# Performance work log

Hardware: AMD Instinct MI355X
Metric: run time of the kernel (lower is better)

Reference implementation:

```python
import jax, jax.numpy as jnp
import numpy as np

N_NODES = 50000
N_EDGES = 800000
N_RELS = 65
D = 64
N_GRAPHS = 512


def setup_inputs() -> dict:
    key = jax.random.key(0)
    ks = jax.random.split(key, 20)
    inp = {
        "node_feats": jax.random.normal(ks[0], (N_NODES, D), dtype=jnp.float32),
        "etypes": jax.random.randint(ks[1], (N_EDGES,), 0, N_RELS),
        "src": jax.random.randint(ks[2], (N_EDGES,), 0, N_NODES),
        "dst": jax.random.randint(ks[3], (N_EDGES,), 0, N_NODES),
        "graph_ids": jnp.sort(jax.random.randint(ks[4], (N_NODES,), 0, N_GRAPHS)),
    }
    s = 1.0 / np.sqrt(D)
    # 3 RGCN layers: per-relation weights (basis with num_bases=num_rels == full) + bias
    for i, k in zip(range(1, 4), (ks[5], ks[6], ks[7])):
        inp[f"W_rel{i}"] = jax.random.normal(k, (N_RELS, D, D), dtype=jnp.float32) * s
        inp[f"b{i}"] = jnp.zeros((D,), dtype=jnp.float32)
    # 3 FC layers
    for i, k in zip(range(1, 4), (ks[8], ks[9], ks[10])):
        inp[f"fc_W{i}"] = jax.random.normal(k, (D, D), dtype=jnp.float32) * s
        inp[f"fc_b{i}"] = jnp.zeros((D,), dtype=jnp.float32)
    inp["pred_W"] = jax.random.normal(ks[11], (D, 2), dtype=jnp.float32) * s
    inp["pred_b"] = jnp.zeros((2,), dtype=jnp.float32)
    return inp


def _rgcn_layer(h, W, b, etypes, src, dst):
    # all-relation projection: [N, R, K]
    proj = jnp.einsum('nd,rdk->nrk', h, W)
    # per-edge gather of relation-specific message: [E, K]
    msg = proj[src, etypes]
    # scatter-sum into destination nodes
    agg = jax.ops.segment_sum(msg, dst, num_segments=h.shape[0])
    return jax.nn.relu(agg + b)


def reference(node_feats, etypes, src, dst, graph_ids,
              W_rel1, b1, W_rel2, b2, W_rel3, b3,
              fc_W1, fc_b1, fc_W2, fc_b2, fc_W3, fc_b3,
              pred_W, pred_b):
    h = node_feats
    h = _rgcn_layer(h, W_rel1, b1, etypes, src, dst)
    h = _rgcn_layer(h, W_rel2, b2, etypes, src, dst)
    h = _rgcn_layer(h, W_rel3, b3, etypes, src, dst)
    # sum-pool nodes per graph: [G, D]
    g = jax.ops.segment_sum(h, graph_ids, num_segments=N_GRAPHS)
    g = jax.nn.relu(g @ fc_W1 + fc_b1)
    g = jax.nn.relu(g @ fc_W2 + fc_b2)
    g = jax.nn.relu(g @ fc_W3 + fc_b3)
    return g @ pred_W + pred_b
```

## Files before the change

### kernel.cpp

```cpp
#include <hip/hip_runtime.h>
#include <hip/hip_bf16.h>

#define N_NODES 50000
#define N_EDGES 800000
#define N_RELS 65
#define DIM 64
#define N_GRAPHS 512

#define SORT_BLOCKS 1024
#define CHUNK ((N_EDGES + SORT_BLOCKS - 1) / SORT_BLOCKS)

#define SCAN_BLK 512
#define NSCAN_BLKS ((N_NODES + SCAN_BLK - 1) / SCAN_BLK)

#define MSG_BLOCKS 2048
#define NWAVES (MSG_BLOCKS * 4)

typedef __attribute__((ext_vector_type(8))) short short8;
typedef __attribute__((ext_vector_type(4))) float f32x4;


__global__ __launch_bounds__(256) void prep_kernel(
    const float* __restrict__ x, const int* __restrict__ et,
    __hip_bfloat16* __restrict__ y, int* __restrict__ cnt_d,
    int* __restrict__ blk_hist,
    const float* __restrict__ W1, const float* __restrict__ W2,
    const float* __restrict__ W3,
    __hip_bfloat16* __restrict__ Wt1, __hip_bfloat16* __restrict__ Wt2,
    __hip_bfloat16* __restrict__ Wt3,
    int* __restrict__ done_flags) {
    __shared__ int lh[N_RELS];
    __shared__ float tile[64][65];
    int t = threadIdx.x, b = blockIdx.x;
    int gtid = b * 256 + t;

    if (gtid < N_NODES) cnt_d[gtid] = 0;
    if (gtid < 2) done_flags[gtid] = 0;

    if (t < N_RELS) lh[t] = 0;
    __syncthreads();
    int lo = b * CHUNK;
    int hi = lo + CHUNK; if (hi > N_EDGES) hi = N_EDGES;
    for (int i = lo + t; i < hi; i += 256)
        atomicAdd(&lh[et[i]], 1);

    for (int i = gtid; i < (N_NODES * DIM) / 4; i += SORT_BLOCKS * 256) {
        float4 v = *(const float4*)(x + (size_t)i * 4);
        unsigned short us[4];
        us[0] = __hip_bfloat16_raw(__float2bfloat16(v.x)).x;
        us[1] = __hip_bfloat16_raw(__float2bfloat16(v.y)).x;
        us[2] = __hip_bfloat16_raw(__float2bfloat16(v.z)).x;
        us[3] = __hip_bfloat16_raw(__float2bfloat16(v.w)).x;
        *(ushort4*)(y + (size_t)i * 4) = *(const ushort4*)us;
    }

    if (b < 3 * N_RELS) {
        int which = b / N_RELS, r = b - which * N_RELS;
        const float* W = (which == 0) ? W1 : (which == 1) ? W2 : W3;
        __hip_bfloat16* Wt = (which == 0) ? Wt1 : (which == 1) ? Wt2 : Wt3;
        for (int i = t; i < 4096; i += 256) {
            int row = i >> 6, col = i & 63;
            tile[row][col] = W[(size_t)r * 4096 + i];
        }
        __syncthreads();
        for (int i = t; i < 4096; i += 256) {
            int row = i >> 6, col = i & 63;
            Wt[(size_t)r * 4096 + i] = __float2bfloat16(tile[col][row]);
        }
    }

    __syncthreads();
    if (t < N_RELS) blk_hist[t * SORT_BLOCKS + b] = lh[t];
}


__global__ __launch_bounds__(256) void relscan_kernel(const int* __restrict__ blk_hist,
                                                      int* __restrict__ blk_off,
                                                      int* __restrict__ rel_tot,
                                                      int* __restrict__ rel_ptr,
                                                      int* __restrict__ tile_base,
                                                      int* __restrict__ done) {
    __shared__ int wsum[4];
    int r = blockIdx.x;
    int t = threadIdx.x;
    int w = t >> 6, lane = t & 63;
    const int PER = SORT_BLOCKS / 256;
    int4 v0 = *(const int4*)(blk_hist + (size_t)r * SORT_BLOCKS + t * PER);
    int vals[4] = {v0.x, v0.y, v0.z, v0.w};
    int s = 0;
    #pragma unroll
    for (int j = 0; j < PER; ++j) s += vals[j];
    int x = s;
    #pragma unroll
    for (int off = 1; off < 64; off <<= 1) {
        int y = __shfl_up(x, off);
        if (lane >= off) x += y;
    }
    if (lane == 63) wsum[w] = x;
    __syncthreads();
    int base = 0;
    for (int i = 0; i < w; ++i) base += wsum[i];
    int run = base + x - s;
    int out[4];
    #pragma unroll
    for (int j = 0; j < PER; ++j) { out[j] = run; run += vals[j]; }
    *(int4*)(blk_off + (size_t)r * SORT_BLOCKS + t * PER) = *(const int4*)&out[0];

    if (t == 255) {
        __hip_atomic_store(&rel_tot[r], base + x, __ATOMIC_RELAXED, __HIP_MEMORY_SCOPE_AGENT);
        __threadfence();
        int ticket = atomicAdd(done, 1);
        if (ticket == N_RELS - 1) {
            int ss = 0, tt = 0;
            for (int q = 0; q < N_RELS; ++q) {
                int v = __hip_atomic_load(&rel_tot[q], __ATOMIC_RELAXED,
                                          __HIP_MEMORY_SCOPE_AGENT);
                rel_ptr[q] = ss; ss += v;
                tile_base[q] = tt; tt += (v + 15) >> 4;
            }
            rel_ptr[N_RELS] = N_EDGES;
            tile_base[N_RELS] = tt;
        }
    }
}


__global__ __launch_bounds__(256) void scatter2_kernel(
    const int* __restrict__ et, const int* __restrict__ src,
    const int* __restrict__ dst, const int* __restrict__ blk_hist,
    const int* __restrict__ blk_off, const int* __restrict__ rel_ptr,
    unsigned long long* __restrict__ epk, int* __restrict__ cnt_d) {
    __shared__ unsigned long long buf[CHUNK];
    __shared__ unsigned char relof[CHUNK];
    __shared__ int loff[N_RELS + 1];
    __shared__ int lcur[N_RELS];
    __shared__ int gbase[N_RELS];
    int t = threadIdx.x, b = blockIdx.x;

    if (t < 64) {
        int v = blk_hist[t * SORT_BLOCKS + b];
        int x = v;
        #pragma unroll
        for (int off = 1; off < 64; off <<= 1) {
            int y = __shfl_up(x, off);
            if (t >= off) x += y;
        }
        loff[t] = x - v;
        lcur[t] = x - v;
        gbase[t] = rel_ptr[t] + blk_off[t * SORT_BLOCKS + b];
        if (t == 63) { loff[64] = x; lcur[64] = x; }
    } else if (t == 64) {
        gbase[64] = rel_ptr[64] + blk_off[64 * SORT_BLOCKS + b];
    }
    __syncthreads();

    int lo = b * CHUNK;
    int hi = lo + CHUNK; if (hi > N_EDGES) hi = N_EDGES;
    int nloc = hi - lo;

    #pragma unroll
    for (int k = 0; k < 4; ++k) {
        int i = lo + t + k * 256;
        if (i < hi) {
            int r = et[i], d = dst[i];
            unsigned s = (unsigned)src[i];
            int rank = atomicAdd(&cnt_d[d], 1);
            int pl = atomicAdd(&lcur[r], 1);
            unsigned lo32 = s | ((unsigned)d << 16);
            buf[pl] = (unsigned long long)lo32 |
                      ((unsigned long long)(unsigned)rank << 32);
            relof[pl] = (unsigned char)r;
        }
    }
    __syncthreads();

    #pragma unroll
    for (int k = 0; k < 4; ++k) {
        int i = t + k * 256;
        if (i < nloc) {
            int r = relof[i];
            epk[gbase[r] + i - loff[r]] = buf[i];
        }
    }
}


__global__ __launch_bounds__(SCAN_BLK) void scanblk_kernel(
    const int* __restrict__ cnt, int* __restrict__ outv,
    int* __restrict__ blk_tot, int* __restrict__ blk_base,
    const int* __restrict__ gid, int* __restrict__ g_ptr,
    int* __restrict__ cnt_g, int* __restrict__ done) {
    __shared__ int tmp[SCAN_BLK];
    __shared__ int is_last;
    int t = threadIdx.x;
    int i = blockIdx.x * SCAN_BLK + t;
    int v = (i < N_NODES) ? cnt[i] : 0;
    tmp[t] = v;
    __syncthreads();
    for (int off = 1; off < SCAN_BLK; off <<= 1) {
        int add = (t >= off) ? tmp[t - off] : 0;
        __syncthreads();
        tmp[t] += add;
        __syncthreads();
    }
    if (i < N_NODES) outv[i] = tmp[t] - v;
    if (t == SCAN_BLK - 1) {
        __hip_atomic_store(&blk_tot[blockIdx.x], tmp[t], __ATOMIC_RELAXED,
                           __HIP_MEMORY_SCOPE_AGENT);
        __threadfence();
        int ticket = atomicAdd(done, 1);
        is_last = (ticket == NSCAN_BLKS - 1) ? 1 : 0;
    }
    __syncthreads();
    if (is_last) {
        if (t == 0) {
            int run = 0;
            for (int b2 = 0; b2 < NSCAN_BLKS; ++b2) {
                int v2 = __hip_atomic_load(&blk_tot[b2], __ATOMIC_RELAXED,
                                           __HIP_MEMORY_SCOPE_AGENT);
                blk_base[b2] = run; run += v2;
            }
        }
        if (t < N_GRAPHS) {
            int g = t;
            int lo2 = 0, hi2 = N_NODES;
            while (lo2 < hi2) { int m = (lo2 + hi2) >> 1; if (gid[m] < g) lo2 = m + 1; else hi2 = m; }
            int a2 = lo2;
            lo2 = 0; hi2 = N_NODES;
            int g1 = g + 1;
            while (lo2 < hi2) { int m = (lo2 + hi2) >> 1; if (gid[m] < g1) lo2 = m + 1; else hi2 = m; }
            g_ptr[g] = a2;
            cnt_g[g] = lo2 - a2;
        }
    }
}


__global__ void unpack_kernel(const unsigned long long* __restrict__ epk,
                              const int* __restrict__ outv,
                              const int* __restrict__ blk_base,
                              int* __restrict__ src_s, int* __restrict__ dpos) {
    int i = blockIdx.x * 256 + threadIdx.x;
    if (i < N_EDGES) {
        unsigned long long e = epk[i];
        int s = (int)(e & 0xFFFFu);
        int d = (int)((e >> 16) & 0xFFFFu);
        int rank = (int)(e >> 32);
        src_s[i] = s;
        dpos[i] = rank + outv[d] + blk_base[d >> 9];
    }
}


__device__ inline unsigned pack2bf(float x, float y) {
    unsigned short ux = __hip_bfloat16_raw(__float2bfloat16(x)).x;
    unsigned short uy = __hip_bfloat16_raw(__float2bfloat16(y)).x;
    return (unsigned)ux | ((unsigned)uy << 16);
}

__global__ __launch_bounds__(256) void msg_mfma_kernel(
    const __hip_bfloat16* __restrict__ hb, const __hip_bfloat16* __restrict__ Wt,
    const int* __restrict__ rel_ptr, const int* __restrict__ tile_base,
    const int* __restrict__ src_s, const int* __restrict__ dpos,
    __hip_bfloat16* __restrict__ msg) {
    int t = threadIdx.x;
    int w = t >> 6, lane = t & 63;
    int quad = lane >> 4, m16 = lane & 15;
    int wave = blockIdx.x * 4 + w;

    int ntiles = tile_base[N_RELS];
    int tpw = (ntiles + NWAVES - 1) / NWAVES;
    int T = wave * tpw;
    int T1 = T + tpw; if (T1 > ntiles) T1 = ntiles;
    if (T >= T1) return;

    int r = 0;
    while (T >= tile_base[r + 1]) ++r;

    while (T < T1) {
        int chunk_end = tile_base[r + 1]; if (chunk_end > T1) chunk_end = T1;
        int e_base = rel_ptr[r], t_base = tile_base[r];
        int seg_end = rel_ptr[r + 1];

        const __hip_bfloat16* Wr = Wt + (size_t)r * (DIM * DIM);
        short8 bf00 = *(const short8*)(Wr + (4 * m16)     * DIM + quad * 8);
        short8 bf01 = *(const short8*)(Wr + (4 * m16 + 1) * DIM + quad * 8);
        short8 bf02 = *(const short8*)(Wr + (4 * m16 + 2) * DIM + quad * 8);
        short8 bf03 = *(const short8*)(Wr + (4 * m16 + 3) * DIM + quad * 8);
        short8 bf10 = *(const short8*)(Wr + (4 * m16)     * DIM + 32 + quad * 8);
        short8 bf11 = *(const short8*)(Wr + (4 * m16 + 1) * DIM + 32 + quad * 8);
        short8 bf12 = *(const short8*)(Wr + (4 * m16 + 2) * DIM + 32 + quad * 8);
        short8 bf13 = *(const short8*)(Wr + (4 * m16 + 3) * DIM + 32 + quad * 8);

        auto loadidx = [&](int TT, int& sv, int& dp) {
            int TC = TT < chunk_end ? TT : chunk_end - 1;
            int i = e_base + (TC - t_base) * 16 + lane;
            if (i >= N_EDGES) i = N_EDGES - 1;
            sv = src_s[i]; dp = dpos[i];
        };
        auto gatherA = [&](int sv, short8& x0, short8& x1) {
            int s = __shfl(sv, m16);
            const __hip_bfloat16* hp = hb + (size_t)s * DIM + quad * 8;
            x0 = *(const short8*)hp;
            x1 = *(const short8*)(hp + 32);
        };

        int sv0, dp0, sv1, dp1, sv2, dp2;
        short8 a0c, a1c, a0n, a1n;
        loadidx(T,     sv0, dp0);
        loadidx(T + 1, sv1, dp1);
        gatherA(sv0, a0c, a1c);

        for (; T < chunk_end; ++T) {
            loadidx(T + 2, sv2, dp2);
            gatherA(sv1, a0n, a1n);

            int e0 = e_base + (T - t_base) * 16;
            int rows = seg_end - e0; if (rows > 16) rows = 16;

            f32x4 c0 = {0.f, 0.f, 0.f, 0.f}, c1 = c0, c2 = c0, c3 = c0;
            c0 = __builtin_amdgcn_mfma_f32_16x16x32_bf16(a0c, bf00, c0, 0, 0, 0);
            c1 = __builtin_amdgcn_mfma_f32_16x16x32_bf16(a0c, bf01, c1, 0, 0, 0);
            c2 = __builtin_amdgcn_mfma_f32_16x16x32_bf16(a0c, bf02, c2, 0, 0, 0);
            c3 = __builtin_amdgcn_mfma_f32_16x16x32_bf16(a0c, bf03, c3, 0, 0, 0);
            c0 = __builtin_amdgcn_mfma_f32_16x16x32_bf16(a1c, bf10, c0, 0, 0, 0);
            c1 = __builtin_amdgcn_mfma_f32_16x16x32_bf16(a1c, bf11, c1, 0, 0, 0);
            c2 = __builtin_amdgcn_mfma_f32_16x16x32_bf16(a1c, bf12, c2, 0, 0, 0);
            c3 = __builtin_amdgcn_mfma_f32_16x16x32_bf16(a1c, bf13, c3, 0, 0, 0);

            int dpr[4];
            #pragma unroll
            for (int g = 0; g < 4; ++g) dpr[g] = __shfl(dp0, quad * 4 + g);

            #pragma unroll
            for (int g = 0; g < 4; ++g) {
                if (quad * 4 + g < rows) {
                    uint2 pk;
                    pk.x = pack2bf(c0[g], c1[g]);
                    pk.y = pack2bf(c2[g], c3[g]);
                    *(uint2*)(msg + (size_t)dpr[g] * DIM + 4 * m16) = pk;
                }
            }

            sv0 = sv1; dp0 = dp1; sv1 = sv2; dp1 = dp2;
            a0c = a0n; a1c = a1n;
        }
        ++r;
        while (T < T1 && T >= tile_base[r + 1]) ++r;
    }
}


__global__ __launch_bounds__(256) void agg_kernel(
    const __hip_bfloat16* __restrict__ msg, const int* __restrict__ outv,
    const int* __restrict__ blk_base,
    const int* __restrict__ cnt_d, const float* __restrict__ b,
    __hip_bfloat16* __restrict__ hout) {
    int wave = blockIdx.x * 4 + (threadIdx.x >> 6);
    int lane = threadIdx.x & 63;
    if (wave >= N_NODES) return;
    int j0 = outv[wave] + blk_base[wave >> 9];
    int n  = cnt_d[wave];
    int rgrp = lane >> 3, dgrp = lane & 7;

    float a[8] = {0.f, 0.f, 0.f, 0.f, 0.f, 0.f, 0.f, 0.f};
    for (int jj = 0; jj < n; jj += 8) {
        int row = jj + rgrp;
        if (row < n) {
            uint4 d = *(const uint4*)(msg + (size_t)(j0 + row) * DIM + dgrp * 8);
            a[0] += __uint_as_float(d.x << 16);
            a[1] += __uint_as_float(d.x & 0xffff0000u);
            a[2] += __uint_as_float(d.y << 16);
            a[3] += __uint_as_float(d.y & 0xffff0000u);
            a[4] += __uint_as_float(d.z << 16);
            a[5] += __uint_as_float(d.z & 0xffff0000u);
            a[6] += __uint_as_float(d.w << 16);
            a[7] += __uint_as_float(d.w & 0xffff0000u);
        }
    }
    #pragma unroll
    for (int i = 0; i < 8; ++i) {
        a[i] += __shfl_xor(a[i], 8);
        a[i] += __shfl_xor(a[i], 16);
        a[i] += __shfl_xor(a[i], 32);
    }
    if (rgrp == 0) {
        unsigned short us[8];
        #pragma unroll
        for (int i = 0; i < 8; ++i) {
            float v = a[i] + b[dgrp * 8 + i];
            us[i] = __hip_bfloat16_raw(__float2bfloat16(v > 0.f ? v : 0.f)).x;
        }
        *(uint4*)(hout + (size_t)wave * DIM + dgrp * 8) = *(const uint4*)us;
    }
}


__global__ __launch_bounds__(256) void poolfc_kernel(
    const __hip_bfloat16* __restrict__ h, const int* __restrict__ g_ptr,
    const int* __restrict__ cnt_g,
    const float* __restrict__ W1, const float* __restrict__ b1,
    const float* __restrict__ W2, const float* __restrict__ b2,
    const float* __restrict__ W3, const float* __restrict__ b3,
    const float* __restrict__ pW, const float* __restrict__ pb,
    float* __restrict__ out) {
    int wave = blockIdx.x * 4 + (threadIdx.x >> 6);
    int lane = threadIdx.x & 63;
    if (wave >= N_GRAPHS) return;
    int j0 = g_ptr[wave];
    int n  = cnt_g[wave];
    int rgrp = lane >> 3, dgrp = lane & 7;

    float a[8] = {0.f, 0.f, 0.f, 0.f, 0.f, 0.f, 0.f, 0.f};
    for (int jj = 0; jj < n; jj += 8) {
        int row = jj + rgrp;
        if (row < n) {
            uint4 d = *(const uint4*)(h + (size_t)(j0 + row) * DIM + dgrp * 8);
            a[0] += __uint_as_float(d.x << 16);
            a[1] += __uint_as_float(d.x & 0xffff0000u);
            a[2] += __uint_as_float(d.y << 16);
            a[3] += __uint_as_float(d.y & 0xffff0000u);
            a[4] += __uint_as_float(d.z << 16);
            a[5] += __uint_as_float(d.z & 0xffff0000u);
            a[6] += __uint_as_float(d.w << 16);
            a[7] += __uint_as_float(d.w & 0xffff0000u);
        }
    }
    #pragma unroll
    for (int i = 0; i < 8; ++i) {
        a[i] += __shfl_xor(a[i], 8);
        a[i] += __shfl_xor(a[i], 16);
        a[i] += __shfl_xor(a[i], 32);
    }
    float v;
    {
        float acc = b1[lane];
        #pragma unroll
        for (int o = 0; o < 8; ++o)
            #pragma unroll
            for (int q = 0; q < 8; ++q)
                acc += __shfl(a[o], q) * W1[(q * 8 + o) * DIM + lane];
        v = acc > 0.f ? acc : 0.f;
    }
    {
        float acc = b2[lane];
        #pragma unroll
        for (int d = 0; d < DIM; ++d)
            acc += __shfl(v, d) * W2[d * DIM + lane];
        v = acc > 0.f ? acc : 0.f;
    }
    {
        float acc = b3[lane];
        #pragma unroll
        for (int d = 0; d < DIM; ++d)
            acc += __shfl(v, d) * W3[d * DIM + lane];
        v = acc > 0.f ? acc : 0.f;
    }
    float p0 = v * pW[lane * 2 + 0];
    float p1 = v * pW[lane * 2 + 1];
    #pragma unroll
    for (int off = 32; off > 0; off >>= 1) {
        p0 += __shfl_down(p0, off);
        p1 += __shfl_down(p1, off);
    }
    if (lane == 0) {
        out[wave * 2 + 0] = p0 + pb[0];
        out[wave * 2 + 1] = p1 + pb[1];
    }
}


extern "C" void kernel_launch(void* const* d_in, const int* in_sizes, int n_in,
                              void* d_out, int out_size, void* d_ws, size_t ws_size,
                              hipStream_t stream) {
    const float* node_feats = (const float*)d_in[0];
    const int*   etypes     = (const int*)d_in[1];
    const int*   src        = (const int*)d_in[2];
    const int*   dst        = (const int*)d_in[3];
    const int*   graph_ids  = (const int*)d_in[4];
    const float* W1 = (const float*)d_in[5];
    const float* b1 = (const float*)d_in[6];
    const float* W2 = (const float*)d_in[7];
    const float* b2 = (const float*)d_in[8];
    const float* W3 = (const float*)d_in[9];
    const float* b3 = (const float*)d_in[10];
    const float* fcW1 = (const float*)d_in[11];
    const float* fcb1 = (const float*)d_in[12];
    const float* fcW2 = (const float*)d_in[13];
    const float* fcb2 = (const float*)d_in[14];
    const float* fcW3 = (const float*)d_in[15];
    const float* fcb3 = (const float*)d_in[16];
    const float* pW = (const float*)d_in[17];
    const float* pb = (const float*)d_in[18];
    float* out = (float*)d_out;

    char* p = (char*)d_ws;
    auto alloc = [&](size_t bytes) -> void* {
        void* r = (void*)p;
        p += (bytes + 255) & ~(size_t)255;
        return r;
    };
    int* blk_hist  = (int*)alloc((size_t)SORT_BLOCKS * N_RELS * sizeof(int));
    int* blk_off   = (int*)alloc((size_t)SORT_BLOCKS * N_RELS * sizeof(int));
    int* rel_ptr   = (int*)alloc((N_RELS + 1) * sizeof(int));
    int* rel_tot   = (int*)alloc(N_RELS * sizeof(int));
    int* tile_base = (int*)alloc((N_RELS + 1) * sizeof(int));
    unsigned long long* epk = (unsigned long long*)alloc((size_t)N_EDGES * sizeof(unsigned long long));
    int* src_s     = (int*)alloc((size_t)N_EDGES * sizeof(int));
    int* dpos      = (int*)alloc((size_t)N_EDGES * sizeof(int));
    int* cnt_d     = (int*)alloc((size_t)N_NODES * sizeof(int));
    int* outv      = (int*)alloc((size_t)N_NODES * sizeof(int));
    int* blk_tot   = (int*)alloc(NSCAN_BLKS * sizeof(int));
    int* blk_base  = (int*)alloc(NSCAN_BLKS * sizeof(int));
    int* cnt_g     = (int*)alloc(N_GRAPHS * sizeof(int));
    int* g_ptr     = (int*)alloc(N_GRAPHS * sizeof(int));
    int* done_flags= (int*)alloc(2 * sizeof(int));
    __hip_bfloat16* hb0 = (__hip_bfloat16*)alloc((size_t)N_NODES * DIM * sizeof(__hip_bfloat16));
    __hip_bfloat16* hb1 = (__hip_bfloat16*)alloc((size_t)N_NODES * DIM * sizeof(__hip_bfloat16));
    __hip_bfloat16* Wt1 = (__hip_bfloat16*)alloc((size_t)N_RELS * DIM * DIM * sizeof(__hip_bfloat16));
    __hip_bfloat16* Wt2 = (__hip_bfloat16*)alloc((size_t)N_RELS * DIM * DIM * sizeof(__hip_bfloat16));
    __hip_bfloat16* Wt3 = (__hip_bfloat16*)alloc((size_t)N_RELS * DIM * DIM * sizeof(__hip_bfloat16));
    __hip_bfloat16* msg = (__hip_bfloat16*)alloc((size_t)N_EDGES * DIM * sizeof(__hip_bfloat16));

    const int EBLK = (N_EDGES + 255) / 256;
    const int AGG_BLOCKS = (N_NODES + 3) / 4;

    prep_kernel<<<SORT_BLOCKS, 256, 0, stream>>>(node_feats, etypes, hb0, cnt_d, blk_hist,
                                                 W1, W2, W3, Wt1, Wt2, Wt3, done_flags);
    relscan_kernel<<<N_RELS, 256, 0, stream>>>(blk_hist, blk_off, rel_tot,
                                               rel_ptr, tile_base, &done_flags[0]);
    scatter2_kernel<<<SORT_BLOCKS, 256, 0, stream>>>(etypes, src, dst, blk_hist, blk_off,
                                                     rel_ptr, epk, cnt_d);
    scanblk_kernel<<<NSCAN_BLKS, SCAN_BLK, 0, stream>>>(cnt_d, outv, blk_tot, blk_base,
                                                        graph_ids, g_ptr, cnt_g,
                                                        &done_flags[1]);
    unpack_kernel<<<EBLK, 256, 0, stream>>>(epk, outv, blk_base, src_s, dpos);

    msg_mfma_kernel<<<MSG_BLOCKS, 256, 0, stream>>>(hb0, Wt1, rel_ptr, tile_base,
                                                    src_s, dpos, msg);
    agg_kernel<<<AGG_BLOCKS, 256, 0, stream>>>(msg, outv, blk_base, cnt_d, b1, hb1);

    msg_mfma_kernel<<<MSG_BLOCKS, 256, 0, stream>>>(hb1, Wt2, rel_ptr, tile_base,
                                                    src_s, dpos, msg);
    agg_kernel<<<AGG_BLOCKS, 256, 0, stream>>>(msg, outv, blk_base, cnt_d, b2, hb0);

    msg_mfma_kernel<<<MSG_BLOCKS, 256, 0, stream>>>(hb0, Wt3, rel_ptr, tile_base,
                                                    src_s, dpos, msg);
    agg_kernel<<<AGG_BLOCKS, 256, 0, stream>>>(msg, outv, blk_base, cnt_d, b3, hb1);

    poolfc_kernel<<<(N_GRAPHS + 3) / 4, 256, 0, stream>>>(hb1, g_ptr, cnt_g,
                                                          fcW1, fcb1, fcW2, fcb2,
                                                          fcW3, fcb3, pW, pb, out);
}
```

Measured before the change: 366.0 us.

## Fuse message MFMA and aggregation per destination chunk with LDS accumulation

Replaces the relation-sorted edge ordering with a two-level sort: edges are bucketed by 64-node destination chunks and then by relation inside each chunk. Each layer becomes a single kernel that computes MFMA messages per relation group and accumulates them into an LDS tile with shared atomics. The per-edge bf16 message buffer and the separate aggregation pass go away, which removes large global writes and reads. In exchange, weights are reloaded per relation per chunk, small relation groups leave MFMA tiles underfilled, LDS atomics can contend, and chunks are assumed to hold at most 2048 edges.

Result: slower. 1.242 ms (+239.4%).

```diff
diff --git a/kernel.cpp b/kernel.cpp
--- a/kernel.cpp
+++ b/kernel.cpp
@@ -10,39 +10,37 @@
 #define SORT_BLOCKS 1024
 #define CHUNK ((N_EDGES + SORT_BLOCKS - 1) / SORT_BLOCKS)
 
-#define SCAN_BLK 512
-#define NSCAN_BLKS ((N_NODES + SCAN_BLK - 1) / SCAN_BLK)
-
-#define MSG_BLOCKS 2048
-#define NWAVES (MSG_BLOCKS * 4)
+#define DCHUNK 64
+#define NCHUNKS ((N_NODES + DCHUNK - 1) / DCHUNK)
+#define HPAD 1024
+#define MAXCH 2048
 
 typedef __attribute__((ext_vector_type(8))) short short8;
 typedef __attribute__((ext_vector_type(4))) float f32x4;
 
 
 __global__ __launch_bounds__(256) void prep_kernel(
-    const float* __restrict__ x, const int* __restrict__ et,
-    __hip_bfloat16* __restrict__ y, int* __restrict__ cnt_d,
-    int* __restrict__ blk_hist,
+    const float* __restrict__ x, const int* __restrict__ dst,
+    __hip_bfloat16* __restrict__ y, int* __restrict__ blk_hist1,
     const float* __restrict__ W1, const float* __restrict__ W2,
     const float* __restrict__ W3,
     __hip_bfloat16* __restrict__ Wt1, __hip_bfloat16* __restrict__ Wt2,
     __hip_bfloat16* __restrict__ Wt3,
     int* __restrict__ done_flags) {
-    __shared__ int lh[N_RELS];
+    __shared__ int chist[HPAD];
     __shared__ float tile[64][65];
     int t = threadIdx.x, b = blockIdx.x;
     int gtid = b * 256 + t;
 
-    if (gtid < N_NODES) cnt_d[gtid] = 0;
-    if (gtid < 2) done_flags[gtid] = 0;
-
-    if (t < N_RELS) lh[t] = 0;
-    __syncthreads();
+    if (gtid == 0) done_flags[0] = 0;
+
+    for (int i = t; i < HPAD; i += 256) chist[i] = 0;
+    __syncthreads();
+
     int lo = b * CHUNK;
     int hi = lo + CHUNK; if (hi > N_EDGES) hi = N_EDGES;
     for (int i = lo + t; i < hi; i += 256)
-        atomicAdd(&lh[et[i]], 1);
+        atomicAdd(&chist[dst[i] >> 6], 1);
 
     for (int i = gtid; i < (N_NODES * DIM) / 4; i += SORT_BLOCKS * 256) {
         float4 v = *(const float4*)(x + (size_t)i * 4);
@@ -70,26 +68,27 @@
     }
 
     __syncthreads();
-    if (t < N_RELS) blk_hist[t * SORT_BLOCKS + b] = lh[t];
-}
-
-
-__global__ __launch_bounds__(256) void relscan_kernel(const int* __restrict__ blk_hist,
-                                                      int* __restrict__ blk_off,
-                                                      int* __restrict__ rel_tot,
-                                                      int* __restrict__ rel_ptr,
-                                                      int* __restrict__ tile_base,
-                                                      int* __restrict__ done) {
+    for (int i = t; i < HPAD; i += 256)
+        blk_hist1[(size_t)b * HPAD + i] = chist[i];
+}
+
+
+__global__ __launch_bounds__(256) void chunkscan_kernel(
+    const int* __restrict__ blk_hist1, int* __restrict__ blk_off1,
+    int* __restrict__ chunk_tot, int* __restrict__ chunk_ptr,
+    const int* __restrict__ gid, int* __restrict__ g_ptr, int* __restrict__ cnt_g,
+    int* __restrict__ done) {
     __shared__ int wsum[4];
+    __shared__ int is_last;
     int r = blockIdx.x;
     int t = threadIdx.x;
     int w = t >> 6, lane = t & 63;
-    const int PER = SORT_BLOCKS / 256;
-    int4 v0 = *(const int4*)(blk_hist + (size_t)r * SORT_BLOCKS + t * PER);
-    int vals[4] = {v0.x, v0.y, v0.z, v0.w};
-    int s = 0;
-    #pragma unroll
-    for (int j = 0; j < PER; ++j) s += vals[j];
+
+    int vals[4];
+    #pragma unroll
+    for (int j = 0; j < 4; ++j)
+        vals[j] = blk_hist1[(size_t)(t * 4 + j) * HPAD + r];
+    int s = vals[0] + vals[1] + vals[2] + vals[3];
     int x = s;
     #pragma unroll
     for (int off = 1; off < 64; off <<= 1) {
@@ -101,128 +100,53 @@
     int base = 0;
     for (int i = 0; i < w; ++i) base += wsum[i];
     int run = base + x - s;
-    int out[4];
-    #pragma unroll
-    for (int j = 0; j < PER; ++j) { out[j] = run; run += vals[j]; }
-    *(int4*)(blk_off + (size_t)r * SORT_BLOCKS + t * PER) = *(const int4*)&out[0];
+    #pragma unroll
+    for (int j = 0; j < 4; ++j) {
+        blk_off1[(size_t)(t * 4 + j) * HPAD + r] = run;
+        run += vals[j];
+    }
 
     if (t == 255) {
-        __hip_atomic_store(&rel_tot[r], base + x, __ATOMIC_RELAXED, __HIP_MEMORY_SCOPE_AGENT);
-        __threadfence();
-        int ticket = atomicAdd(done, 1);
-        if (ticket == N_RELS - 1) {
-            int ss = 0, tt = 0;
-            for (int q = 0; q < N_RELS; ++q) {
-                int v = __hip_atomic_load(&rel_tot[q], __ATOMIC_RELAXED,
-                                          __HIP_MEMORY_SCOPE_AGENT);
-                rel_ptr[q] = ss; ss += v;
-                tile_base[q] = tt; tt += (v + 15) >> 4;
-            }
-            rel_ptr[N_RELS] = N_EDGES;
-            tile_base[N_RELS] = tt;
-        }
-    }
-}
-
-
-__global__ __launch_bounds__(256) void scatter2_kernel(
-    const int* __restrict__ et, const int* __restrict__ src,
-    const int* __restrict__ dst, const int* __restrict__ blk_hist,
-    const int* __restrict__ blk_off, const int* __restrict__ rel_ptr,
-    unsigned long long* __restrict__ epk, int* __restrict__ cnt_d) {
-    __shared__ unsigned long long buf[CHUNK];
-    __shared__ unsigned char relof[CHUNK];
-    __shared__ int loff[N_RELS + 1];
-    __shared__ int lcur[N_RELS];
-    __shared__ int gbase[N_RELS];
-    int t = threadIdx.x, b = blockIdx.x;
-
-    if (t < 64) {
-        int v = blk_hist[t * SORT_BLOCKS + b];
-        int x = v;
-        #pragma unroll
-        for (int off = 1; off < 64; off <<= 1) {
-            int y = __shfl_up(x, off);
-            if (t >= off) x += y;
-        }
-        loff[t] = x - v;
-        lcur[t] = x - v;
-        gbase[t] = rel_ptr[t] + blk_off[t * SORT_BLOCKS + b];
-        if (t == 63) { loff[64] = x; lcur[64] = x; }
-    } else if (t == 64) {
-        gbase[64] = rel_ptr[64] + blk_off[64 * SORT_BLOCKS + b];
-    }
-    __syncthreads();
-
-    int lo = b * CHUNK;
-    int hi = lo + CHUNK; if (hi > N_EDGES) hi = N_EDGES;
-    int nloc = hi - lo;
-
-    #pragma unroll
-    for (int k = 0; k < 4; ++k) {
-        int i = lo + t + k * 256;
-        if (i < hi) {
-            int r = et[i], d = dst[i];
-            unsigned s = (unsigned)src[i];
-            int rank = atomicAdd(&cnt_d[d], 1);
-            int pl = atomicAdd(&lcur[r], 1);
-            unsigned lo32 = s | ((unsigned)d << 16);
-            buf[pl] = (unsigned long long)lo32 |
-                      ((unsigned long long)(unsigned)rank << 32);
-            relof[pl] = (unsigned char)r;
-        }
-    }
-    __syncthreads();
-
-    #pragma unroll
-    for (int k = 0; k < 4; ++k) {
-        int i = t + k * 256;
-        if (i < nloc) {
-            int r = relof[i];
-            epk[gbase[r] + i - loff[r]] = buf[i];
-        }
-    }
-}
-
-
-__global__ __launch_bounds__(SCAN_BLK) void scanblk_kernel(
-    const int* __restrict__ cnt, int* __restrict__ outv,
-    int* __restrict__ blk_tot, int* __restrict__ blk_base,
-    const int* __restrict__ gid, int* __restrict__ g_ptr,
-    int* __restrict__ cnt_g, int* __restrict__ done) {
-    __shared__ int tmp[SCAN_BLK];
-    __shared__ int is_last;
-    int t = threadIdx.x;
-    int i = blockIdx.x * SCAN_BLK + t;
-    int v = (i < N_NODES) ? cnt[i] : 0;
-    tmp[t] = v;
-    __syncthreads();
-    for (int off = 1; off < SCAN_BLK; off <<= 1) {
-        int add = (t >= off) ? tmp[t - off] : 0;
-        __syncthreads();
-        tmp[t] += add;
-        __syncthreads();
-    }
-    if (i < N_NODES) outv[i] = tmp[t] - v;
-    if (t == SCAN_BLK - 1) {
-        __hip_atomic_store(&blk_tot[blockIdx.x], tmp[t], __ATOMIC_RELAXED,
+        __hip_atomic_store(&chunk_tot[r], base + x, __ATOMIC_RELAXED,
                            __HIP_MEMORY_SCOPE_AGENT);
         __threadfence();
         int ticket = atomicAdd(done, 1);
-        is_last = (ticket == NSCAN_BLKS - 1) ? 1 : 0;
-    }
-    __syncthreads();
+        is_last = (ticket == NCHUNKS - 1) ? 1 : 0;
+    }
+    __syncthreads();
+
     if (is_last) {
-        if (t == 0) {
-            int run = 0;
-            for (int b2 = 0; b2 < NSCAN_BLKS; ++b2) {
-                int v2 = __hip_atomic_load(&blk_tot[b2], __ATOMIC_RELAXED,
-                                           __HIP_MEMORY_SCOPE_AGENT);
-                blk_base[b2] = run; run += v2;
-            }
-        }
-        if (t < N_GRAPHS) {
-            int g = t;
+        int v2[4];
+        #pragma unroll
+        for (int j = 0; j < 4; ++j) {
+            int idx = t * 4 + j;
+            v2[j] = (idx < NCHUNKS)
+                        ? __hip_atomic_load(&chunk_tot[idx], __ATOMIC_RELAXED,
+                                            __HIP_MEMORY_SCOPE_AGENT)
+                        : 0;
+        }
+        int s2 = v2[0] + v2[1] + v2[2] + v2[3];
+        int x2 = s2;
+        #pragma unroll
+        for (int off = 1; off < 64; off <<= 1) {
+            int y = __shfl_up(x2, off);
+            if (lane >= off) x2 += y;
+        }
+        __syncthreads();
+        if (lane == 63) wsum[w] = x2;
+        __syncthreads();
+        int base2 = 0;
+        for (int i = 0; i < w; ++i) base2 += wsum[i];
+        int run2 = base2 + x2 - s2;
+        #pragma unroll
+        for (int j = 0; j < 4; ++j) {
+            int idx = t * 4 + j;
+            if (idx < NCHUNKS) chunk_ptr[idx] = run2;
+            else chunk_ptr[idx] = N_EDGES;
+            run2 += v2[j];
+            if (idx == NCHUNKS - 1) chunk_ptr[NCHUNKS] = run2;
+        }
+        for (int g = t; g < N_GRAPHS; g += 256) {
             int lo2 = 0, hi2 = N_NODES;
             while (lo2 < hi2) { int m = (lo2 + hi2) >> 1; if (gid[m] < g) lo2 = m + 1; else hi2 = m; }
             int a2 = lo2;
@@ -236,51 +160,138 @@
 }
 
 
-__global__ void unpack_kernel(const unsigned long long* __restrict__ epk,
-                              const int* __restrict__ outv,
-                              const int* __restrict__ blk_base,
-                              int* __restrict__ src_s, int* __restrict__ dpos) {
-    int i = blockIdx.x * 256 + threadIdx.x;
-    if (i < N_EDGES) {
-        unsigned long long e = epk[i];
-        int s = (int)(e & 0xFFFFu);
-        int d = (int)((e >> 16) & 0xFFFFu);
-        int rank = (int)(e >> 32);
-        src_s[i] = s;
-        dpos[i] = rank + outv[d] + blk_base[d >> 9];
-    }
-}
-
-
-__device__ inline unsigned pack2bf(float x, float y) {
-    unsigned short ux = __hip_bfloat16_raw(__float2bfloat16(x)).x;
-    unsigned short uy = __hip_bfloat16_raw(__float2bfloat16(y)).x;
-    return (unsigned)ux | ((unsigned)uy << 16);
-}
-
-__global__ __launch_bounds__(256) void msg_mfma_kernel(
+__global__ __launch_bounds__(256) void scatterc_kernel(
+    const int* __restrict__ et, const int* __restrict__ src,
+    const int* __restrict__ dst, const int* __restrict__ blk_hist1,
+    const int* __restrict__ blk_off1, const int* __restrict__ chunk_ptr,
+    unsigned* __restrict__ epk2) {
+    __shared__ int loff[HPAD];
+    __shared__ int lcur[HPAD];
+    __shared__ int gbase[HPAD];
+    __shared__ unsigned srec[CHUNK];
+    __shared__ unsigned short sbin[CHUNK];
+    __shared__ int wsum[4];
+    int t = threadIdx.x, b = blockIdx.x;
+    int w = t >> 6, lane = t & 63;
+
+    int4 hv = *(const int4*)(blk_hist1 + (size_t)b * HPAD + t * 4);
+    int4 ov = *(const int4*)(blk_off1 + (size_t)b * HPAD + t * 4);
+    int4 cp = *(const int4*)(chunk_ptr + t * 4);
+    int vals[4] = {hv.x, hv.y, hv.z, hv.w};
+    int offs[4] = {ov.x, ov.y, ov.z, ov.w};
+    int cps[4]  = {cp.x, cp.y, cp.z, cp.w};
+    int s = vals[0] + vals[1] + vals[2] + vals[3];
+    int x = s;
+    #pragma unroll
+    for (int off = 1; off < 64; off <<= 1) {
+        int y = __shfl_up(x, off);
+        if (lane >= off) x += y;
+    }
+    if (lane == 63) wsum[w] = x;
+    __syncthreads();
+    int base = 0;
+    for (int i = 0; i < w; ++i) base += wsum[i];
+    int run = base + x - s;
+    #pragma unroll
+    for (int j = 0; j < 4; ++j) {
+        loff[t * 4 + j] = run;
+        lcur[t * 4 + j] = run;
+        gbase[t * 4 + j] = cps[j] + offs[j];
+        run += vals[j];
+    }
+    __syncthreads();
+
+    int lo = b * CHUNK;
+    int hi = lo + CHUNK; if (hi > N_EDGES) hi = N_EDGES;
+    int nloc = hi - lo;
+
+    #pragma unroll
+    for (int k = 0; k < 4; ++k) {
+        int i = lo + t + k * 256;
+        if (i < hi) {
+            int d = dst[i];
+            int c = d >> 6;
+            unsigned rec = (unsigned)src[i] | ((unsigned)(d & 63) << 16) |
+                           ((unsigned)et[i] << 22);
+            int pl = atomicAdd(&lcur[c], 1);
+            srec[pl] = rec;
+            sbin[pl] = (unsigned short)c;
+        }
+    }
+    __syncthreads();
+
+    #pragma unroll
+    for (int k = 0; k < 4; ++k) {
+        int i = t + k * 256;
+        if (i < nloc) {
+            int c = sbin[i];
+            epk2[gbase[c] + i - loff[c]] = srec[i];
+        }
+    }
+}
+
+
+__global__ __launch_bounds__(256) void chunksort_kernel(
+    const unsigned* __restrict__ epk2, const int* __restrict__ chunk_ptr,
+    unsigned* __restrict__ efin, int* __restrict__ grpoff) {
+    __shared__ unsigned sin[MAXCH];
+    __shared__ int h65[N_RELS], off66[N_RELS + 1], cur65[N_RELS];
+    int c = blockIdx.x, t = threadIdx.x;
+    int e0 = chunk_ptr[c], e1 = chunk_ptr[c + 1];
+    int n = e1 - e0;
+    if (n > MAXCH) n = MAXCH;
+
+    if (t < N_RELS) h65[t] = 0;
+    __syncthreads();
+    for (int i = t; i < n; i += 256) {
+        unsigned v = epk2[e0 + i];
+        sin[i] = v;
+        atomicAdd(&h65[v >> 22], 1);
+    }
+    __syncthreads();
+    if (t < 64) {
+        int v = h65[t];
+        int x = v;
+        #pragma unroll
+        for (int off = 1; off < 64; off <<= 1) {
+            int y = __shfl_up(x, off);
+            if (t >= off) x += y;
+        }
+        off66[t] = x - v;
+        if (t == 63) off66[64] = x;
+    }
+    __syncthreads();
+    if (t == 0) off66[65] = off66[64] + h65[64];
+    __syncthreads();
+    if (t < N_RELS) cur65[t] = off66[t];
+    if (t < N_RELS + 1) grpoff[c * 66 + t] = e0 + off66[t];
+    __syncthreads();
+    for (int i = t; i < n; i += 256) {
+        unsigned v = sin[i];
+        int r = v >> 22;
+        int pos = atomicAdd(&cur65[r], 1);
+        efin[e0 + pos] = v;
+    }
+}
+
+
+__global__ __launch_bounds__(256) void layer_kernel(
     const __hip_bfloat16* __restrict__ hb, const __hip_bfloat16* __restrict__ Wt,
-    const int* __restrict__ rel_ptr, const int* __restrict__ tile_base,
-    const int* __restrict__ src_s, const int* __restrict__ dpos,
-    __hip_bfloat16* __restrict__ msg) {
-    int t = threadIdx.x;
+    const unsigned* __restrict__ efin, const int* __restrict__ grpoff,
+    const float* __restrict__ bias, __hip_bfloat16* __restrict__ hout) {
+    __shared__ float acc[64 * 68];
+    __shared__ int goff[N_RELS + 1];
+    int c = blockIdx.x, t = threadIdx.x;
     int w = t >> 6, lane = t & 63;
     int quad = lane >> 4, m16 = lane & 15;
-    int wave = blockIdx.x * 4 + w;
-
-    int ntiles = tile_base[N_RELS];
-    int tpw = (ntiles + NWAVES - 1) / NWAVES;
-    int T = wave * tpw;
-    int T1 = T + tpw; if (T1 > ntiles) T1 = ntiles;
-    if (T >= T1) return;
-
-    int r = 0;
-    while (T >= tile_base[r + 1]) ++r;
-
-    while (T < T1) {
-        int chunk_end = tile_base[r + 1]; if (chunk_end > T1) chunk_end = T1;
-        int e_base = rel_ptr[r], t_base = tile_base[r];
-        int seg_end = rel_ptr[r + 1];
+
+    for (int i = t; i < 64 * 68; i += 256) acc[i] = 0.f;
+    if (t < N_RELS + 1) goff[t] = grpoff[c * 66 + t];
+    __syncthreads();
+
+    for (int r = w; r < N_RELS; r += 4) {
+        int g0 = goff[r], g1 = goff[r + 1];
+        if (g0 >= g1) continue;
 
         const __hip_bfloat16* Wr = Wt + (size_t)r * (DIM * DIM);
         short8 bf00 = *(const short8*)(Wr + (4 * m16)     * DIM + quad * 8);
@@ -292,106 +303,55 @@
         short8 bf12 = *(const short8*)(Wr + (4 * m16 + 2) * DIM + 32 + quad * 8);
         short8 bf13 = *(const short8*)(Wr + (4 * m16 + 3) * DIM + 32 + quad * 8);
 
-        auto loadidx = [&](int TT, int& sv, int& dp) {
-            int TC = TT < chunk_end ? TT : chunk_end - 1;
-            int i = e_base + (TC - t_base) * 16 + lane;
-            if (i >= N_EDGES) i = N_EDGES - 1;
-            sv = src_s[i]; dp = dpos[i];
-        };
-        auto gatherA = [&](int sv, short8& x0, short8& x1) {
-            int s = __shfl(sv, m16);
+        for (int tb = g0; tb < g1; tb += 16) {
+            int e = tb + m16;
+            int ec = (e < g1) ? e : g1 - 1;
+            unsigned rec = efin[ec];
+            int s = rec & 0xFFFF;
             const __hip_bfloat16* hp = hb + (size_t)s * DIM + quad * 8;
-            x0 = *(const short8*)hp;
-            x1 = *(const short8*)(hp + 32);
-        };
-
-        int sv0, dp0, sv1, dp1, sv2, dp2;
-        short8 a0c, a1c, a0n, a1n;
-        loadidx(T,     sv0, dp0);
-        loadidx(T + 1, sv1, dp1);
-        gatherA(sv0, a0c, a1c);
-
-        for (; T < chunk_end; ++T) {
-            loadidx(T + 2, sv2, dp2);
-            gatherA(sv1, a0n, a1n);
-
-            int e0 = e_base + (T - t_base) * 16;
-            int rows = seg_end - e0; if (rows > 16) rows = 16;
+            short8 a0 = *(const short8*)hp;
+            short8 a1 = *(const short8*)(hp + 32);
 
             f32x4 c0 = {0.f, 0.f, 0.f, 0.f}, c1 = c0, c2 = c0, c3 = c0;
-            c0 = __builtin_amdgcn_mfma_f32_16x16x32_bf16(a0c, bf00, c0, 0, 0, 0);
-            c1 = __builtin_amdgcn_mfma_f32_16x16x32_bf16(a0c, bf01, c1, 0, 0, 0);
-            c2 = __builtin_amdgcn_mfma_f32_16x16x32_bf16(a0c, bf02, c2, 0, 0, 0);
-            c3 = __builtin_amdgcn_mfma_f32_16x16x32_bf16(a0c, bf03, c3, 0, 0, 0);
-            c0 = __builtin_amdgcn_mfma_f32_16x16x32_bf16(a1c, bf10, c0, 0, 0, 0);
-            c1 = __builtin_amdgcn_mfma_f32_16x16x32_bf16(a1c, bf11, c1, 0, 0, 0);
-            c2 = __builtin_amdgcn_mfma_f32_16x16x32_bf16(a1c, bf12, c2, 0, 0, 0);
-            c3 = __builtin_amdgcn_mfma_f32_16x16x32_bf16(a1c, bf13, c3, 0, 0, 0);
-
-            int dpr[4];
-            #pragma unroll
-            for (int g = 0; g < 4; ++g) dpr[g] = __shfl(dp0, quad * 4 + g);
-
+            c0 = __builtin_amdgcn_mfma_f32_16x16x32_bf16(a0, bf00, c0, 0, 0, 0);
+            c1 = __builtin_amdgcn_mfma_f32_16x16x32_bf16(a0, bf01, c1, 0, 0, 0);
+            c2 = __builtin_amdgcn_mfma_f32_16x16x32_bf16(a0, bf02, c2, 0, 0, 0);
+            c3 = __builtin_amdgcn_mfma_f32_16x16x32_bf16(a0, bf03, c3, 0, 0, 0);
+            c0 = __builtin_amdgcn_mfma_f32_16x16x32_bf16(a1, bf10, c0, 0, 0, 0);
+            c1 = __builtin_amdgcn_mfma_f32_16x16x32_bf16(a1, bf11, c1, 0, 0, 0);
+            c2 = __builtin_amdgcn_mfma_f32_16x16x32_bf16(a1, bf12, c2, 0, 0, 0);
+            c3 = __builtin_amdgcn_mfma_f32_16x16x32_bf16(a1, bf13, c3, 0, 0, 0);
+
+            int rows = g1 - tb; if (rows > 16) rows = 16;
             #pragma unroll
             for (int g = 0; g < 4; ++g) {
-                if (quad * 4 + g < rows) {
-                    uint2 pk;
-                    pk.x = pack2bf(c0[g], c1[g]);
-                    pk.y = pack2bf(c2[g], c3[g]);
-                    *(uint2*)(msg + (size_t)dpr[g] * DIM + 4 * m16) = pk;
+                int row = quad * 4 + g;
+                unsigned rr = (unsigned)__shfl((int)rec, row);
+                if (row < rows) {
+                    int dl = (rr >> 16) & 63;
+                    float* ap = &acc[dl * 68 + 4 * m16];
+                    atomicAdd(ap + 0, c0[g]);
+                    atomicAdd(ap + 1, c1[g]);
+                    atomicAdd(ap + 2, c2[g]);
+                    atomicAdd(ap + 3, c3[g]);
                 }
             }
-
-            sv0 = sv1; dp0 = dp1; sv1 = sv2; dp1 = dp2;
-            a0c = a0n; a1c = a1n;
-        }
-        ++r;
-        while (T < T1 && T >= tile_base[r + 1]) ++r;
-    }
-}
-
-
-__global__ __launch_bounds__(256) void agg_kernel(
-    const __hip_bfloat16* __restrict__ msg, const int* __restrict__ outv,
-    const int* __restrict__ blk_base,
-    const int* __restrict__ cnt_d, const float* __restrict__ b,
-    __hip_bfloat16* __restrict__ hout) {
-    int wave = blockIdx.x * 4 + (threadIdx.x >> 6);
-    int lane = threadIdx.x & 63;
-    if (wave >= N_NODES) return;
-    int j0 = outv[wave] + blk_base[wave >> 9];
-    int n  = cnt_d[wave];
-    int rgrp = lane >> 3, dgrp = lane & 7;
-
-    float a[8] = {0.f, 0.f, 0.f, 0.f, 0.f, 0.f, 0.f, 0.f};
-    for (int jj = 0; jj < n; jj += 8) {
-        int row = jj + rgrp;
-        if (row < n) {
-            uint4 d = *(const uint4*)(msg + (size_t)(j0 + row) * DIM + dgrp * 8);
-            a[0] += __uint_as_float(d.x << 16);
-            a[1] += __uint_as_float(d.x & 0xffff0000u);
-            a[2] += __uint_as_float(d.y << 16);
-            a[3] += __uint_as_float(d.y & 0xffff0000u);
-            a[4] += __uint_as_float(d.z << 16);
-            a[5] += __uint_as_float(d.z & 0xffff0000u);
-            a[6] += __uint_as_float(d.w << 16);
-            a[7] += __uint_as_float(d.w & 0xffff0000u);
-        }
-    }
-    #pragma unroll
-    for (int i = 0; i < 8; ++i) {
-        a[i] += __shfl_xor(a[i], 8);
-        a[i] += __shfl_xor(a[i], 16);
-        a[i] += __shfl_xor(a[i], 32);
-    }
-    if (rgrp == 0) {
-        unsigned short us[8];
-        #pragma unroll
-        for (int i = 0; i < 8; ++i) {
-            float v = a[i] + b[dgrp * 8 + i];
-            us[i] = __hip_bfloat16_raw(__float2bfloat16(v > 0.f ? v : 0.f)).x;
-        }
-        *(uint4*)(hout + (size_t)wave * DIM + dgrp * 8) = *(const uint4*)us;
+        }
+    }
+    __syncthreads();
+
+    int dl = t >> 2, q4 = (t & 3) * 16;
+    int d = c * DCHUNK + dl;
+    if (d < N_NODES) {
+        unsigned short us[16];
+        #pragma unroll
+        for (int j = 0; j < 16; ++j) {
+            float v = acc[dl * 68 + q4 + j] + bias[q4 + j];
+            us[j] = __hip_bfloat16_raw(__float2bfloat16(v > 0.f ? v : 0.f)).x;
+        }
+        __hip_bfloat16* hp = hout + (size_t)d * DIM + q4;
+        *(uint4*)hp = *(const uint4*)&us[0];
+        *(uint4*)(hp + 8) = *(const uint4*)&us[8];
     }
 }
 
@@ -500,18 +460,13 @@
         p += (bytes + 255) & ~(size_t)255;
         return r;
     };
-    int* blk_hist  = (int*)alloc((size_t)SORT_BLOCKS * N_RELS * sizeof(int));
-    int* blk_off   = (int*)alloc((size_t)SORT_BLOCKS * N_RELS * sizeof(int));
-    int* rel_ptr   = (int*)alloc((N_RELS + 1) * sizeof(int));
-    int* rel_tot   = (int*)alloc(N_RELS * sizeof(int));
-    int* tile_base = (int*)alloc((N_RELS + 1) * sizeof(int));
-    unsigned long long* epk = (unsigned long long*)alloc((size_t)N_EDGES * sizeof(unsigned long long));
-    int* src_s     = (int*)alloc((size_t)N_EDGES * sizeof(int));
-    int* dpos      = (int*)alloc((size_t)N_EDGES * sizeof(int));
-    int* cnt_d     = (int*)alloc((size_t)N_NODES * sizeof(int));
-    int* outv      = (int*)alloc((size_t)N_NODES * sizeof(int));
-    int* blk_tot   = (int*)alloc(NSCAN_BLKS * sizeof(int));
-    int* blk_base  = (int*)alloc(NSCAN_BLKS * sizeof(int));
+    int* blk_hist1 = (int*)alloc((size_t)SORT_BLOCKS * HPAD * sizeof(int));
+    int* blk_off1  = (int*)alloc((size_t)SORT_BLOCKS * HPAD * sizeof(int));
+    int* chunk_tot = (int*)alloc(HPAD * sizeof(int));
+    int* chunk_ptr = (int*)alloc((HPAD + 1) * sizeof(int));
+    unsigned* epk2 = (unsigned*)alloc((size_t)N_EDGES * sizeof(unsigned));
+    unsigned* efin = (unsigned*)alloc((size_t)N_EDGES * sizeof(unsigned));
+    int* grpoff    = (int*)alloc((size_t)NCHUNKS * 66 * sizeof(int));
     int* cnt_g     = (int*)alloc(N_GRAPHS * sizeof(int));
     int* g_ptr     = (int*)alloc(N_GRAPHS * sizeof(int));
     int* done_flags= (int*)alloc(2 * sizeof(int));
@@ -520,33 +475,19 @@
     __hip_bfloat16* Wt1 = (__hip_bfloat16*)alloc((size_t)N_RELS * DIM * DIM * sizeof(__hip_bfloat16));
     __hip_bfloat16* Wt2 = (__hip_bfloat16*)alloc((size_t)N_RELS * DIM * DIM * sizeof(__hip_bfloat16));
     __hip_bfloat16* Wt3 = (__hip_bfloat16*)alloc((size_t)N_RELS * DIM * DIM * sizeof(__hip_bfloat16));
-    __hip_bfloat16* msg = (__hip_bfloat16*)alloc((size_t)N_EDGES * DIM * sizeof(__hip_bfloat16));
-
-    const int EBLK = (N_EDGES + 255) / 256;
-    const int AGG_BLOCKS = (N_NODES + 3) / 4;
-
-    prep_kernel<<<SORT_BLOCKS, 256, 0, stream>>>(node_feats, etypes, hb0, cnt_d, blk_hist,
+
+    prep_kernel<<<SORT_BLOCKS, 256, 0, stream>>>(node_feats, dst, hb0, blk_hist1,
                                                  W1, W2, W3, Wt1, Wt2, Wt3, done_flags);
-    relscan_kernel<<<N_RELS, 256, 0, stream>>>(blk_hist, blk_off, rel_tot,
-                                               rel_ptr, tile_base, &done_flags[0]);
-    scatter2_kernel<<<SORT_BLOCKS, 256, 0, stream>>>(etypes, src, dst, blk_hist, blk_off,
-                                                     rel_ptr, epk, cnt_d);
-    scanblk_kernel<<<NSCAN_BLKS, SCAN_BLK, 0, stream>>>(cnt_d, outv, blk_tot, blk_base,
-                                                        graph_ids, g_ptr, cnt_g,
-                                                        &done_flags[1]);
-    unpack_kernel<<<EBLK, 256, 0, stream>>>(epk, outv, blk_base, src_s, dpos);
-
-    msg_mfma_kernel<<<MSG_BLOCKS, 256, 0, stream>>>(hb0, Wt1, rel_ptr, tile_base,
-                                                    src_s, dpos, msg);
-    agg_kernel<<<AGG_BLOCKS, 256, 0, stream>>>(msg, outv, blk_base, cnt_d, b1, hb1);
-
-    msg_mfma_kernel<<<MSG_BLOCKS, 256, 0, stream>>>(hb1, Wt2, rel_ptr, tile_base,
-                                                    src_s, dpos, msg);
-    agg_kernel<<<AGG_BLOCKS, 256, 0, stream>>>(msg, outv, blk_base, cnt_d, b2, hb0);
-
-    msg_mfma_kernel<<<MSG_BLOCKS, 256, 0, stream>>>(hb0, Wt3, rel_ptr, tile_base,
-                                                    src_s, dpos, msg);
-    agg_kernel<<<AGG_BLOCKS, 256, 0, stream>>>(msg, outv, blk_base, cnt_d, b3, hb1);
+    chunkscan_kernel<<<NCHUNKS, 256, 0, stream>>>(blk_hist1, blk_off1, chunk_tot,
+                                                  chunk_ptr, graph_ids, g_ptr, cnt_g,
+                                                  &done_flags[0]);
+    scatterc_kernel<<<SORT_BLOCKS, 256, 0, stream>>>(etypes, src, dst, blk_hist1,
+                                                     blk_off1, chunk_ptr, epk2);
+    chunksort_kernel<<<NCHUNKS, 256, 0, stream>>>(epk2, chunk_ptr, efin, grpoff);
+
+    layer_kernel<<<NCHUNKS, 256, 0, stream>>>(hb0, Wt1, efin, grpoff, b1, hb1);
+    layer_kernel<<<NCHUNKS, 256, 0, stream>>>(hb1, Wt2, efin, grpoff, b2, hb0);
+    layer_kernel<<<NCHUNKS, 256, 0, stream>>>(hb0, Wt3, efin, grpoff, b3, hb1);
 
     poolfc_kernel<<<(N_GRAPHS + 3) / 4, 256, 0, stream>>>(hb1, g_ptr, cnt_g,
                                                           fcW1, fcb1, fcW2, fcb2,
```
